# Optimization experiments

Hardware: AMD Instinct MI355X
Metric: run time of the kernel (lower is better)

Reference implementation:

```python
import jax, jax.numpy as jnp
import numpy as np

B, N = 8192, 64
EPS = 1e-3  # diagonal jitter to guarantee strict positive-definiteness


def setup_inputs() -> dict:
    key = jax.random.key(0)
    A = jax.random.normal(key, (B, N, N), dtype=jnp.float32)
    # SPD construction: X = A A^T / N + eps*I  (eigenvalues strictly > 0)
    X = jnp.einsum('bik,bjk->bij', A, A) / N + EPS * jnp.eye(N, dtype=jnp.float32)
    return {"X": X}


def reference(X):
    # sym_logm: eig-based matrix logarithm of batched SPD matrices
    w, v = jnp.linalg.eigh(X)                    # w: [B,N], v: [B,N,N]
    logm = jnp.einsum('bik,bk,bjk->bij', v, jnp.log(w), v)  # V diag(log w) V^T
    # embed with tril=False: flatten from dim 1 -> [B, N*N]
    return logm.reshape(logm.shape[0], -1)
```

## Files before the change

### kernel.cpp

```cpp
#include <hip/hip_runtime.h>
#include <math.h>

#define NSW 12

__device__ __forceinline__ float bperm_f(int addr4, float v) {
    return __int_as_float(__builtin_amdgcn_ds_bpermute(addr4, __float_as_int(v)));
}

__global__ __launch_bounds__(64, 2) void logeig_kernel(
    const float* __restrict__ Xg, float* __restrict__ out)
{
    __shared__ __align__(16) float W[64 * 68];
    __shared__ float hlds[64];

    const int lane = threadIdx.x;
    const int b = blockIdx.x;

    float x[64];
    {
        const float4* __restrict__ Xb4 = (const float4*)(Xg + (size_t)b * 4096);
        #pragma unroll
        for (int m = 0; m < 16; ++m) {
            float4 v = Xb4[lane * 16 + m];
            x[4 * m + 0] = v.x; x[4 * m + 1] = v.y;
            x[4 * m + 2] = v.z; x[4 * m + 3] = v.w;
        }
    }

    float d;
    {
        float a0 = 0.f, a1 = 0.f, a2 = 0.f, a3 = 0.f;
        #pragma unroll
        for (int k = 0; k < 64; k += 4) {
            a0 = fmaf(x[k + 0], x[k + 0], a0);
            a1 = fmaf(x[k + 1], x[k + 1], a1);
            a2 = fmaf(x[k + 2], x[k + 2], a2);
            a3 = fmaf(x[k + 3], x[k + 3], a3);
        }
        d = (a0 + a1) + (a2 + a3);
    }

    const int m  = lane - 1;
    int pm = (lane == 0) ? 0 : ((63 - m) % 63);
    int p0 = 0;

    for (int sweep = 0; sweep < NSW; ++sweep) {
        for (int r = 0; r < 63; ++r) {
            const int prt  = (lane == 0) ? (p0 + 1)
                                         : ((pm == m) ? 0 : (pm + 1));
            const int prt4 = prt << 2;

            float xp[64];
            float g0 = 0.f, g1 = 0.f, g2 = 0.f, g3 = 0.f;
            #pragma unroll
            for (int k = 0; k < 64; k += 4) {
                xp[k + 0] = bperm_f(prt4, x[k + 0]);
                xp[k + 1] = bperm_f(prt4, x[k + 1]);
                xp[k + 2] = bperm_f(prt4, x[k + 2]);
                xp[k + 3] = bperm_f(prt4, x[k + 3]);
                g0 = fmaf(x[k + 0], xp[k + 0], g0);
                g1 = fmaf(x[k + 1], xp[k + 1], g1);
                g2 = fmaf(x[k + 2], xp[k + 2], g2);
                g3 = fmaf(x[k + 3], xp[k + 3], g3);
            }
            const float g  = (g0 + g1) + (g2 + g3);
            const float dq = bperm_f(prt4, d);
            const bool  lo = lane < prt;
            const bool  ok = fabsf(g) > 1e-30f;

            const float num  = lo ? (dq - d) : (d - dq);
            const float zeta = num / (2.f * g);
            const float az   = fabsf(zeta);
            float tl = 1.f / (az + sqrtf(fmaf(az, az, 1.f)));
            tl = (zeta >= 0.f) ? tl : -tl;
            float tn = lo ? tl : -tl;
            tn = ok ? tn : 0.f;
            const float c = rsqrtf(fmaf(tn, tn, 1.f));
            const float s = c * tn;

            d = fmaf(-tn, g, d);

            #pragma unroll
            for (int k = 0; k < 64; ++k)
                x[k] = fmaf(-s, xp[k], c * x[k]);

            pm = (pm + 1 == 63) ? 0 : (pm + 1);
            p0 += 32; if (p0 >= 63) p0 -= 63;
        }

        float a0 = 0.f, a1 = 0.f, a2 = 0.f, a3 = 0.f;
        #pragma unroll
        for (int k = 0; k < 64; k += 4) {
            a0 = fmaf(x[k + 0], x[k + 0], a0);
            a1 = fmaf(x[k + 1], x[k + 1], a1);
            a2 = fmaf(x[k + 2], x[k + 2], a2);
            a3 = fmaf(x[k + 3], x[k + 3], a3);
        }
        d = (a0 + a1) + (a2 + a3);
    }

    const float alpha = fmaxf(d, 1e-12f);
    const float h = 0.5f * logf(alpha) / alpha;
    hlds[lane] = h;
    #pragma unroll
    for (int k = 0; k < 64; ++k) W[k * 68 + lane] = x[k];
    __syncthreads();

    float rreg[64];
    #pragma unroll
    for (int l = 0; l < 64; ++l) rreg[l] = W[lane * 68 + l] * hlds[l];

    float* __restrict__ outb = out + (size_t)b * 4096;
    for (int i = 0; i < 64; ++i) {
        float acc0 = 0.f, acc1 = 0.f;
        #pragma unroll
        for (int l4 = 0; l4 < 16; ++l4) {
            const float4 w4 = *(const float4*)&W[i * 68 + l4 * 4];
            acc0 = fmaf(w4.x, rreg[4 * l4 + 0], acc0);
            acc1 = fmaf(w4.y, rreg[4 * l4 + 1], acc1);
            acc0 = fmaf(w4.z, rreg[4 * l4 + 2], acc0);
            acc1 = fmaf(w4.w, rreg[4 * l4 + 3], acc1);
        }
        outb[i * 64 + lane] = acc0 + acc1;
    }
}

extern "C" void kernel_launch(void* const* d_in, const int* in_sizes, int n_in,
                              void* d_out, int out_size, void* d_ws, size_t ws_size,
                              hipStream_t stream)
{
    const float* X = (const float*)d_in[0];
    float* out = (float*)d_out;
    const int B = in_sizes[0] / 4096;
    logeig_kernel<<<dim3(B), dim3(64), 0, stream>>>(X, out);
}
```

Measured before the change: 5.285 ms.

## Chunk reconstruction through small LDS tile and raise occupancy to three waves

The final V·diag(h)·V^T reconstruction now goes through a 64x20 LDS chunk, staging 16 columns at a time into registers, instead of holding the full 64x68 matrix in LDS. This cuts the shared-memory footprint, and launch bounds are raised to allow three waves per SIMD. An empty asm barrier on xp pins the permuted values in registers and constrains compiler scheduling. The cost is extra syncthreads, a 64-element accumulator array, and tighter register limits that could cause spills in the Jacobi loop.

```diff
diff --git a/kernel.cpp b/kernel.cpp
--- a/kernel.cpp
+++ b/kernel.cpp
@@ -7,10 +7,10 @@
     return __int_as_float(__builtin_amdgcn_ds_bpermute(addr4, __float_as_int(v)));
 }
 
-__global__ __launch_bounds__(64, 2) void logeig_kernel(
+__global__ __launch_bounds__(64, 3) void logeig_kernel(
     const float* __restrict__ Xg, float* __restrict__ out)
 {
-    __shared__ __align__(16) float W[64 * 68];
+    __shared__ __align__(16) float Wc[64 * 20];
     __shared__ float hlds[64];
 
     const int lane = threadIdx.x;
@@ -20,10 +20,10 @@
     {
         const float4* __restrict__ Xb4 = (const float4*)(Xg + (size_t)b * 4096);
         #pragma unroll
-        for (int m = 0; m < 16; ++m) {
-            float4 v = Xb4[lane * 16 + m];
-            x[4 * m + 0] = v.x; x[4 * m + 1] = v.y;
-            x[4 * m + 2] = v.z; x[4 * m + 3] = v.w;
+        for (int q = 0; q < 16; ++q) {
+            float4 v = Xb4[lane * 16 + q];
+            x[4 * q + 0] = v.x; x[4 * q + 1] = v.y;
+            x[4 * q + 2] = v.z; x[4 * q + 3] = v.w;
         }
     }
 
@@ -63,6 +63,9 @@
                 g2 = fmaf(x[k + 2], xp[k + 2], g2);
                 g3 = fmaf(x[k + 3], xp[k + 3], g3);
             }
+            #pragma unroll
+            for (int k = 0; k < 64; ++k) asm volatile("" : "+v"(xp[k]));
+
             const float g  = (g0 + g1) + (g2 + g3);
             const float dq = bperm_f(prt4, d);
             const bool  lo = lane < prt;
@@ -102,27 +105,43 @@
     const float alpha = fmaxf(d, 1e-12f);
     const float h = 0.5f * logf(alpha) / alpha;
     hlds[lane] = h;
+
+    float acc[64];
     #pragma unroll
-    for (int k = 0; k < 64; ++k) W[k * 68 + lane] = x[k];
-    __syncthreads();
+    for (int i = 0; i < 64; ++i) acc[i] = 0.f;
 
-    float rreg[64];
-    #pragma unroll
-    for (int l = 0; l < 64; ++l) rreg[l] = W[lane * 68 + l] * hlds[l];
+    const int cg = lane >> 4;
+    const int cc = lane & 15;
+
+    for (int gi = 0; gi < 4; ++gi) {
+        if (cg == gi) {
+            #pragma unroll
+            for (int k = 0; k < 64; ++k) Wc[k * 20 + cc] = x[k];
+        }
+        __syncthreads();
+
+        float r0[16];
+        #pragma unroll
+        for (int j = 0; j < 16; ++j) r0[j] = Wc[lane * 20 + j] * hlds[gi * 16 + j];
+
+        #pragma unroll
+        for (int i = 0; i < 64; ++i) {
+            const float4 wa = *(const float4*)&Wc[i * 20 + 0];
+            const float4 wb = *(const float4*)&Wc[i * 20 + 4];
+            const float4 wc = *(const float4*)&Wc[i * 20 + 8];
+            const float4 wd = *(const float4*)&Wc[i * 20 + 12];
+            float t0 = fmaf(wa.x, r0[0],  fmaf(wa.y, r0[1],  fmaf(wa.z, r0[2],  wa.w * r0[3])));
+            float t1 = fmaf(wb.x, r0[4],  fmaf(wb.y, r0[5],  fmaf(wb.z, r0[6],  wb.w * r0[7])));
+            float t2 = fmaf(wc.x, r0[8],  fmaf(wc.y, r0[9],  fmaf(wc.z, r0[10], wc.w * r0[11])));
+            float t3 = fmaf(wd.x, r0[12], fmaf(wd.y, r0[13], fmaf(wd.z, r0[14], wd.w * r0[15])));
+            acc[i] += (t0 + t1) + (t2 + t3);
+        }
+        __syncthreads();
+    }
 
     float* __restrict__ outb = out + (size_t)b * 4096;
-    for (int i = 0; i < 64; ++i) {
-        float acc0 = 0.f, acc1 = 0.f;
-        #pragma unroll
-        for (int l4 = 0; l4 < 16; ++l4) {
-            const float4 w4 = *(const float4*)&W[i * 68 + l4 * 4];
-            acc0 = fmaf(w4.x, rreg[4 * l4 + 0], acc0);
-            acc1 = fmaf(w4.y, rreg[4 * l4 + 1], acc1);
-            acc0 = fmaf(w4.z, rreg[4 * l4 + 2], acc0);
-            acc1 = fmaf(w4.w, rreg[4 * l4 + 3], acc1);
-        }
-        outb[i * 64 + lane] = acc0 + acc1;
-    }
+    #pragma unroll
+    for (int i = 0; i < 64; ++i) outb[i * 64 + lane] = acc[i];
 }
 
 extern "C" void kernel_launch(void* const* d_in, const int* in_sizes, int n_in,
```

New measurement: 7.044 ms. 1.33x slower.
